# Kernel tuning notes

Hardware: AMD Instinct MI355X
Metric: run time of the kernel (lower is better)

The kernel has to match this reference:

```python
import jax, jax.numpy as jnp
import numpy as np

N, E, D, H = 100000, 1600000, 128, 2
D2 = D * H  # conv2 output dim = out_dim * heads = 256


def setup_inputs() -> dict:
    key = jax.random.key(0)
    ks = jax.random.split(key, 9)
    x = jax.random.normal(ks[0], (N, D), dtype=jnp.float32)
    edge_index = jax.random.randint(ks[1], (2, E), 0, N, dtype=jnp.int64)
    edge_weight = jax.random.uniform(ks[2], (E,), dtype=jnp.float32)
    s = 1.0 / np.sqrt(D)
    W_rel1 = jax.random.normal(ks[3], (D, D), dtype=jnp.float32) * s
    W_root1 = jax.random.normal(ks[4], (D, D), dtype=jnp.float32) * s
    b1 = jnp.zeros((D,), dtype=jnp.float32)
    W_rel2 = jax.random.normal(ks[5], (D, D2), dtype=jnp.float32) * s
    W_root2 = jax.random.normal(ks[6], (D, D2), dtype=jnp.float32) * s
    b2 = jnp.zeros((D2,), dtype=jnp.float32)
    return {"x": x, "edge_index": edge_index, "edge_weight": edge_weight,
            "W_rel1": W_rel1, "b1": b1, "W_root1": W_root1,
            "W_rel2": W_rel2, "b2": b2, "W_root2": W_root2}


def _graph_conv(x, src, dst, edge_weight, W_rel, b, W_root, n_nodes):
    # message: w_e * x_src ; aggregate: mean over incoming edges at dst
    msgs = x[src] * edge_weight[:, None]                       # [E, D]
    summed = jax.ops.segment_sum(msgs, dst, num_segments=n_nodes)  # [N, D]
    cnt = jax.ops.segment_sum(jnp.ones((src.shape[0],), x.dtype), dst,
                              num_segments=n_nodes)
    mean = summed / jnp.maximum(cnt, 1.0)[:, None]
    # GraphConv: lin_rel(aggr) + lin_root(x); bias only on lin_rel
    return mean @ W_rel + b + x @ W_root


def reference(x, edge_index, edge_weight, W_rel1, b1, W_root1, W_rel2, b2, W_root2):
    src, dst = edge_index[0], edge_index[1]
    n = x.shape[0]
    h = _graph_conv(x, src, dst, edge_weight, W_rel1, b1, W_root1, n)
    out = _graph_conv(h, src, dst, edge_weight, W_rel2, b2, W_root2, n)
    return out
```

## Files before the change

### kernel.cpp

```cpp
#include <hip/hip_runtime.h>
#include <hip/hip_bf16.h>

#define D_IN 128
#define SORT_CHUNK 4096
#define NBUCK 256

typedef __attribute__((ext_vector_type(8))) short bf16x8;
typedef __attribute__((ext_vector_type(8))) unsigned short u16x8;
typedef __attribute__((ext_vector_type(4))) float f32x4;


__global__ __launch_bounds__(256) void scan_block_sums(const int* __restrict__ in,
                                                       int* __restrict__ partial,
                                                       int M) {
    __shared__ int sdata[256];
    int b = blockIdx.x, t = threadIdx.x;
    int base = b * 1024 + t * 4;
    int s = 0;
#pragma unroll
    for (int i = 0; i < 4; ++i) {
        int idx = base + i;
        if (idx < M) s += in[idx];
    }
    sdata[t] = s;
    __syncthreads();
    for (int off = 128; off > 0; off >>= 1) {
        if (t < off) sdata[t] += sdata[t + off];
        __syncthreads();
    }
    if (t == 0) partial[b] = sdata[0];
}

__global__ void scan_partials(int* __restrict__ partial, int nb) {
    if (threadIdx.x == 0 && blockIdx.x == 0) {
        int run = 0;
        for (int i = 0; i < nb; ++i) {
            int t = partial[i];
            partial[i] = run;
            run += t;
        }
    }
}

__global__ __launch_bounds__(256) void scan_final(const int* __restrict__ in,
                                                  const int* __restrict__ partial,
                                                  int* __restrict__ outS,
                                                  int M) {
    __shared__ int sdata[256];
    int b = blockIdx.x, t = threadIdx.x;
    int base = b * 1024 + t * 4;
    int v[4];
    int s = 0;
#pragma unroll
    for (int i = 0; i < 4; ++i) {
        int idx = base + i;
        v[i] = (idx < M) ? in[idx] : 0;
        s += v[i];
    }
    sdata[t] = s;
    __syncthreads();
    for (int o = 1; o < 256; o <<= 1) {
        int tmp = 0;
        if (t >= o) tmp = sdata[t - o];
        __syncthreads();
        sdata[t] += tmp;
        __syncthreads();
    }
    int run = partial[b] + (sdata[t] - s);
#pragma unroll
    for (int i = 0; i < 4; ++i) {
        int idx = base + i;
        if (idx < M) outS[idx] = run;
        run += v[i];
    }
}


__global__ __launch_bounds__(256) void bucket_hist_kernel(const int* __restrict__ dst,
                                                          int* __restrict__ bh,
                                                          long long E, int N, int nbe) {
    __shared__ int cnt[NBUCK];
    cnt[threadIdx.x] = 0;
    __syncthreads();
    long long base = (long long)blockIdx.x * SORT_CHUNK;
    long long end = base + SORT_CHUNK;
    if (end > E) end = E;
    for (long long i = base + threadIdx.x; i < end; i += 256) {
        int b = (int)(((long long)dst[i] << 8) / N);
        atomicAdd(&cnt[b], 1);
    }
    __syncthreads();
    bh[threadIdx.x * nbe + blockIdx.x] = cnt[threadIdx.x];
}

__global__ __launch_bounds__(256) void bucket_scatter_kernel(const int* __restrict__ src,
                                                             const int* __restrict__ dst,
                                                             const float* __restrict__ ew,
                                                             const int* __restrict__ S,
                                                             int2* __restrict__ tmp_edges,
                                                             int* __restrict__ tmp_dst,
                                                             long long E, int N, int nbe) {
    __shared__ int base_lds[NBUCK];
    __shared__ int cnt[NBUCK];
    base_lds[threadIdx.x] = S[threadIdx.x * nbe + blockIdx.x];
    cnt[threadIdx.x] = 0;
    __syncthreads();
    long long b0 = (long long)blockIdx.x * SORT_CHUNK;
    long long e1 = b0 + SORT_CHUNK;
    if (e1 > E) e1 = E;
    for (long long i = b0 + threadIdx.x; i < e1; i += 256) {
        int d = dst[i];
        int b = (int)(((long long)d << 8) / N);
        int p = base_lds[b] + atomicAdd(&cnt[b], 1);
        tmp_edges[p] = make_int2(src[i], __float_as_int(ew[i]));
        tmp_dst[p] = d;
    }
}

__global__ __launch_bounds__(256) void bucket_sort_kernel(const int* __restrict__ S,
                                                          const int2* __restrict__ tmp_edges,
                                                          const int* __restrict__ tmp_dst,
                                                          int2* __restrict__ edges,
                                                          int* __restrict__ hist,
                                                          int* __restrict__ off,
                                                          long long E, int N, int nbe) {
    __shared__ int cnt[512];
    __shared__ int tsum[256];
    __shared__ int pos[512];
    const int b = blockIdx.x, t = threadIdx.x;
    const int lo = (int)(((long long)b * N + 255) >> 8);
    const int hi = (int)(((long long)(b + 1) * N + 255) >> 8);
    const int start = S[b * nbe];
    const int end = (b == NBUCK - 1) ? (int)E : S[(b + 1) * nbe];

    cnt[t] = 0;
    cnt[t + 256] = 0;
    __syncthreads();
    for (int i = start + t; i < end; i += 256)
        atomicAdd(&cnt[tmp_dst[i] - lo], 1);
    __syncthreads();

    int a0 = cnt[2 * t], a1 = cnt[2 * t + 1];
    tsum[t] = a0 + a1;
    __syncthreads();
    for (int o = 1; o < 256; o <<= 1) {
        int v = (t >= o) ? tsum[t - o] : 0;
        __syncthreads();
        tsum[t] += v;
        __syncthreads();
    }
    int excl = tsum[t] - (a0 + a1);
    pos[2 * t]     = start + excl;
    pos[2 * t + 1] = start + excl + a0;

    int d0 = lo + 2 * t, d1 = lo + 2 * t + 1;
    if (d0 < hi) { hist[d0] = a0; off[d0] = start + excl + a0; }
    if (d1 < hi) { hist[d1] = a1; off[d1] = start + excl + a0 + a1; }
    __syncthreads();

    for (int i = start + t; i < end; i += 256) {
        int d = tmp_dst[i] - lo;
        int r = atomicAdd(&pos[d], 1);
        edges[r] = tmp_edges[i];
    }
}


__global__ __launch_bounds__(256) void conv_x_kernel(const float* __restrict__ x,
                                                     __hip_bfloat16* __restrict__ xb,
                                                     long long total4) {
    long long i = (long long)blockIdx.x * 256 + threadIdx.x;
    if (i >= total4) return;
    float4 v = reinterpret_cast<const float4*>(x)[i];
    union { ushort4 u; __hip_bfloat162 h2[2]; } o;
    o.h2[0] = __float22bfloat162_rn(make_float2(v.x, v.y));
    o.h2[1] = __float22bfloat162_rn(make_float2(v.z, v.w));
    reinterpret_cast<ushort4*>(xb)[i] = o.u;
}

template <int DOUT>
__global__ __launch_bounds__(256) void conv_w_kernel(const float* __restrict__ Wrel,
                                                     const float* __restrict__ Wroot,
                                                     __hip_bfloat16* __restrict__ Wt) {
    int idx = blockIdx.x * 256 + threadIdx.x;
    if (idx >= DOUT * 256) return;
    int j = idx >> 8;
    int k = idx & 255;
    float v = (k < 128) ? Wrel[(size_t)k * DOUT + j] : Wroot[(size_t)(k - 128) * DOUT + j];
    Wt[idx] = __float2bfloat16(v);
}

__global__ __launch_bounds__(256) void aggregate_kernel(const __hip_bfloat16* __restrict__ featb,
                                                        const int2* __restrict__ edges,
                                                        const int* __restrict__ off,
                                                        const int* __restrict__ hist,
                                                        __hip_bfloat16* __restrict__ aggb,
                                                        int N) {
    int node = blockIdx.x * 4 + (threadIdx.x >> 6);
    if (node >= N) return;
    const int lane = threadIdx.x & 63;
    const int g = lane >> 4;
    const int sub = lane & 15;
    const int cnt = hist[node];
    const int end = off[node];
    const int start = end - cnt;
    const float inv = 1.0f / fmaxf((float)cnt, 1.0f);

    const ushort* fb = (const ushort*)featb;
    float acc[8] = {0.f, 0.f, 0.f, 0.f, 0.f, 0.f, 0.f, 0.f};

    int e = start + g;
    for (; e + 4 < end; e += 8) {
        int2 e0 = edges[e];
        int2 e1 = edges[e + 4];
        float w0 = __int_as_float(e0.y);
        float w1 = __int_as_float(e1.y);
        u16x8 r0 = *reinterpret_cast<const u16x8*>(fb + (size_t)e0.x * 128 + sub * 8);
        u16x8 r1 = *reinterpret_cast<const u16x8*>(fb + (size_t)e1.x * 128 + sub * 8);
#pragma unroll
        for (int j = 0; j < 8; ++j) {
            acc[j] += w0 * __int_as_float((unsigned)r0[j] << 16)
                    + w1 * __int_as_float((unsigned)r1[j] << 16);
        }
    }
    if (e < end) {
        int2 e0 = edges[e];
        float w0 = __int_as_float(e0.y);
        u16x8 r0 = *reinterpret_cast<const u16x8*>(fb + (size_t)e0.x * 128 + sub * 8);
#pragma unroll
        for (int j = 0; j < 8; ++j)
            acc[j] += w0 * __int_as_float((unsigned)r0[j] << 16);
    }

#pragma unroll
    for (int j = 0; j < 8; ++j) {
        acc[j] += __shfl_xor(acc[j], 16, 64);
        acc[j] += __shfl_xor(acc[j], 32, 64);
    }

    if (g == 0) {
        union { u16x8 u; __hip_bfloat162 h2[4]; } o;
#pragma unroll
        for (int j = 0; j < 4; ++j)
            o.h2[j] = __float22bfloat162_rn(make_float2(acc[2 * j] * inv, acc[2 * j + 1] * inv));
        *reinterpret_cast<u16x8*>((ushort*)aggb + (size_t)node * 128 + sub * 8) = o.u;
    }
}

template <int DOUT, bool OUT_BF16>
__global__ __launch_bounds__(256) void gemm_mfma2(const __hip_bfloat16* __restrict__ Arel,
                                                  const __hip_bfloat16* __restrict__ Aroot,
                                                  const __hip_bfloat16* __restrict__ Wt,
                                                  const float* __restrict__ bias,
                                                  void* __restrict__ outp,
                                                  int M) {
    constexpr int NY = DOUT / 128;
    const int nb = gridDim.x;
    const int orig = blockIdx.x;
    const int xcd = orig & 7;
    const int lid = orig >> 3;
    const int q = nb >> 3, r = nb & 7;
    const int wgid = (xcd < r ? xcd * (q + 1) : r * (q + 1) + (xcd - r) * q) + lid;

    const int ty = wgid % NY;
    const int tx = wgid / NY;
    const int tid = threadIdx.x;
    const int lane = tid & 63;
    const int wave = tid >> 6;
    const int lr = lane & 15;
    const int lk = lane >> 4;
    const int mbase = tx * 128 + (wave >> 1) * 64;
    const int nbase = ty * 128 + (wave & 1) * 64;

    const short* arow[4];
    const short* xrow[4];
#pragma unroll
    for (int mi = 0; mi < 4; ++mi) {
        int row = mbase + mi * 16 + lr;
        int rc = row < M ? row : M - 1;
        arow[mi] = (const short*)Arel  + (size_t)rc * 128 + lk * 8;
        xrow[mi] = (const short*)Aroot + (size_t)rc * 128 + lk * 8;
    }
    const short* wrow[4];
#pragma unroll
    for (int ni = 0; ni < 4; ++ni)
        wrow[ni] = (const short*)Wt + (size_t)(nbase + ni * 16 + lr) * 256 + lk * 8;

    f32x4 zero = {0.f, 0.f, 0.f, 0.f};
    f32x4 acc[4][4];
#pragma unroll
    for (int mi = 0; mi < 4; ++mi)
#pragma unroll
        for (int ni = 0; ni < 4; ++ni) acc[mi][ni] = zero;

#pragma unroll
    for (int kk = 0; kk < 8; ++kk) {
        bf16x8 a[4], b[4];
#pragma unroll
        for (int mi = 0; mi < 4; ++mi)
            a[mi] = (kk < 4)
                ? *reinterpret_cast<const bf16x8*>(arow[mi] + kk * 32)
                : *reinterpret_cast<const bf16x8*>(xrow[mi] + (kk - 4) * 32);
#pragma unroll
        for (int ni = 0; ni < 4; ++ni)
            b[ni] = *reinterpret_cast<const bf16x8*>(wrow[ni] + kk * 32);
#pragma unroll
        for (int mi = 0; mi < 4; ++mi)
#pragma unroll
            for (int ni = 0; ni < 4; ++ni)
                acc[mi][ni] = __builtin_amdgcn_mfma_f32_16x16x32_bf16(a[mi], b[ni], acc[mi][ni], 0, 0, 0);
    }

#pragma unroll
    for (int mi = 0; mi < 4; ++mi)
#pragma unroll
        for (int ni = 0; ni < 4; ++ni) {
            int col = nbase + ni * 16 + lr;
            float bv = bias[col];
#pragma unroll
            for (int rr = 0; rr < 4; ++rr) {
                int row = mbase + mi * 16 + lk * 4 + rr;
                if (row < M) {
                    float v = acc[mi][ni][rr] + bv;
                    if (OUT_BF16)
                        ((__hip_bfloat16*)outp)[(size_t)row * DOUT + col] = __float2bfloat16(v);
                    else
                        __builtin_nontemporal_store(v, (float*)outp + (size_t)row * DOUT + col);
                }
            }
        }
}


extern "C" void kernel_launch(void* const* d_in, const int* in_sizes, int n_in,
                              void* d_out, int out_size, void* d_ws, size_t ws_size,
                              hipStream_t stream) {
    const float* x      = (const float*)d_in[0];
    const int*   ei     = (const int*)d_in[1];
    const float* ew     = (const float*)d_in[2];
    const float* Wrel1  = (const float*)d_in[3];
    const float* b1     = (const float*)d_in[4];
    const float* Wroot1 = (const float*)d_in[5];
    const float* Wrel2  = (const float*)d_in[6];
    const float* b2     = (const float*)d_in[7];
    const float* Wroot2 = (const float*)d_in[8];
    float* out = (float*)d_out;

    const int N = in_sizes[0] / D_IN;
    const long long E = in_sizes[2];
    const int* src = ei;
    const int* dst = ei + E;

    const int nbe = (int)((E + SORT_CHUNK - 1) / SORT_CHUNK);
    const int M = nbe * NBUCK;
    const int nbM = (M + 1023) / 1024;

    int* hist = (int*)d_ws;
    int* off  = hist + N;
    int* part = off + N;
    int2* edges = (int2*)(part + 128);
    __hip_bfloat16* agg1b = (__hip_bfloat16*)(edges + E);
    __hip_bfloat16* xb    = agg1b + (size_t)N * D_IN;
    __hip_bfloat16* agg2b = xb    + (size_t)N * D_IN;
    __hip_bfloat16* hb    = agg2b + (size_t)N * D_IN;
    __hip_bfloat16* Wt1   = hb    + (size_t)N * D_IN;
    __hip_bfloat16* Wt2   = Wt1   + 128 * 256;

    int* bh      = (int*)agg1b;
    int* S       = bh + M;
    int* tmp_dst = S + M;
    int2* tmp_edges = (int2*)agg2b;

    bucket_hist_kernel<<<nbe, 256, 0, stream>>>(dst, bh, E, N, nbe);
    scan_block_sums<<<nbM, 256, 0, stream>>>(bh, part, M);
    scan_partials<<<1, 64, 0, stream>>>(part, nbM);
    scan_final<<<nbM, 256, 0, stream>>>(bh, part, S, M);
    bucket_scatter_kernel<<<nbe, 256, 0, stream>>>(src, dst, ew, S, tmp_edges, tmp_dst, E, N, nbe);
    bucket_sort_kernel<<<NBUCK, 256, 0, stream>>>(S, tmp_edges, tmp_dst, edges, hist, off, E, N, nbe);

    {
        long long total4 = (long long)N * D_IN / 4;
        conv_x_kernel<<<(int)((total4 + 255) / 256), 256, 0, stream>>>(x, xb, total4);
        conv_w_kernel<128><<<(128 * 256 + 255) / 256, 256, 0, stream>>>(Wrel1, Wroot1, Wt1);
        conv_w_kernel<256><<<(256 * 256 + 255) / 256, 256, 0, stream>>>(Wrel2, Wroot2, Wt2);
    }

    const int ab = (N + 3) / 4;
    const int gx = (N + 127) / 128;

    aggregate_kernel<<<ab, 256, 0, stream>>>(xb, edges, off, hist, agg1b, N);
    gemm_mfma2<128, true><<<gx * 1, 256, 0, stream>>>(agg1b, xb, Wt1, b1, hb, N);

    aggregate_kernel<<<ab, 256, 0, stream>>>(hb, edges, off, hist, agg2b, N);
    gemm_mfma2<256, false><<<gx * 2, 256, 0, stream>>>(agg2b, hb, Wt2, b2, out, N);
}
```

Before: 331.6 us.

## Stage GEMM weight tile in swizzled LDS and prefetch all A fragments

The GEMM kernel now copies its 128-column weight slice (64 KB) into shared memory with direct global-to-LDS loads, using an XOR swizzle to avoid bank conflicts, and reads B fragments from LDS instead of from global memory per wave. It also loads all eight K-steps of A fragments into registers before the MFMA loop so the loads can be issued together. In exchange, each block needs 64 KB of LDS and many more registers, which may cap occupancy at two blocks per CU as the launch bound states.

Result: faster. 300.0 us (-9.5%).

```diff
diff --git a/kernel.cpp b/kernel.cpp
--- a/kernel.cpp
+++ b/kernel.cpp
@@ -248,13 +248,15 @@
 }
 
 template <int DOUT, bool OUT_BF16>
-__global__ __launch_bounds__(256) void gemm_mfma2(const __hip_bfloat16* __restrict__ Arel,
-                                                  const __hip_bfloat16* __restrict__ Aroot,
-                                                  const __hip_bfloat16* __restrict__ Wt,
-                                                  const float* __restrict__ bias,
-                                                  void* __restrict__ outp,
-                                                  int M) {
+__global__ __launch_bounds__(256, 2) void gemm_mfma4(const __hip_bfloat16* __restrict__ Arel,
+                                                     const __hip_bfloat16* __restrict__ Aroot,
+                                                     const __hip_bfloat16* __restrict__ Wt,
+                                                     const float* __restrict__ bias,
+                                                     void* __restrict__ outp,
+                                                     int M) {
     constexpr int NY = DOUT / 128;
+    __shared__ __align__(16) unsigned char Bs[65536];
+
     const int nb = gridDim.x;
     const int orig = blockIdx.x;
     const int xcd = orig & 7;
@@ -269,8 +271,23 @@
     const int wave = tid >> 6;
     const int lr = lane & 15;
     const int lk = lane >> 4;
+
+    const char* wbase = (const char*)(Wt + (size_t)ty * 128 * 256);
+#pragma unroll
+    for (int i = 0; i < 16; ++i) {
+        int s = i * 256 + tid;
+        int col = s >> 5;
+        int off16 = s & 31;
+        int g16 = col * 32 + (off16 ^ (col & 7));
+        __builtin_amdgcn_global_load_lds(
+            (const __attribute__((address_space(1))) unsigned int*)(wbase + (size_t)g16 * 16),
+            (__attribute__((address_space(3))) unsigned int*)(&Bs[s * 16]),
+            16, 0, 0);
+    }
+
     const int mbase = tx * 128 + (wave >> 1) * 64;
-    const int nbase = ty * 128 + (wave & 1) * 64;
+    const int nwave = (wave & 1) * 64;
+    const int nbase = ty * 128 + nwave;
 
     const short* arow[4];
     const short* xrow[4];
@@ -281,10 +298,17 @@
         arow[mi] = (const short*)Arel  + (size_t)rc * 128 + lk * 8;
         xrow[mi] = (const short*)Aroot + (size_t)rc * 128 + lk * 8;
     }
-    const short* wrow[4];
-#pragma unroll
-    for (int ni = 0; ni < 4; ++ni)
-        wrow[ni] = (const short*)Wt + (size_t)(nbase + ni * 16 + lr) * 256 + lk * 8;
+
+    __syncthreads();
+
+    bf16x8 abuf[8][4];
+#pragma unroll
+    for (int kk = 0; kk < 8; ++kk)
+#pragma unroll
+        for (int mi = 0; mi < 4; ++mi)
+            abuf[kk][mi] = (kk < 4)
+                ? *reinterpret_cast<const bf16x8*>(arow[mi] + kk * 32)
+                : *reinterpret_cast<const bf16x8*>(xrow[mi] + (kk - 4) * 32);
 
     f32x4 zero = {0.f, 0.f, 0.f, 0.f};
     f32x4 acc[4][4];
@@ -295,20 +319,18 @@
 
 #pragma unroll
     for (int kk = 0; kk < 8; ++kk) {
-        bf16x8 a[4], b[4];
+        bf16x8 b[4];
+#pragma unroll
+        for (int ni = 0; ni < 4; ++ni) {
+            int c = nwave + ni * 16 + lr;
+            int byteoff = c * 512 + ((kk * 64 + lk * 16) ^ ((c & 7) << 4));
+            b[ni] = *reinterpret_cast<const bf16x8*>(&Bs[byteoff]);
+        }
 #pragma unroll
         for (int mi = 0; mi < 4; ++mi)
-            a[mi] = (kk < 4)
-                ? *reinterpret_cast<const bf16x8*>(arow[mi] + kk * 32)
-                : *reinterpret_cast<const bf16x8*>(xrow[mi] + (kk - 4) * 32);
-#pragma unroll
-        for (int ni = 0; ni < 4; ++ni)
-            b[ni] = *reinterpret_cast<const bf16x8*>(wrow[ni] + kk * 32);
-#pragma unroll
-        for (int mi = 0; mi < 4; ++mi)
 #pragma unroll
             for (int ni = 0; ni < 4; ++ni)
-                acc[mi][ni] = __builtin_amdgcn_mfma_f32_16x16x32_bf16(a[mi], b[ni], acc[mi][ni], 0, 0, 0);
+                acc[mi][ni] = __builtin_amdgcn_mfma_f32_16x16x32_bf16(abuf[kk][mi], b[ni], acc[mi][ni], 0, 0, 0);
     }
 
 #pragma unroll
@@ -389,8 +411,8 @@
     const int gx = (N + 127) / 128;
 
     aggregate_kernel<<<ab, 256, 0, stream>>>(xb, edges, off, hist, agg1b, N);
-    gemm_mfma2<128, true><<<gx * 1, 256, 0, stream>>>(agg1b, xb, Wt1, b1, hb, N);
+    gemm_mfma4<128, true><<<gx * 1, 256, 0, stream>>>(agg1b, xb, Wt1, b1, hb, N);
 
     aggregate_kernel<<<ab, 256, 0, stream>>>(hb, edges, off, hist, agg2b, N);
-    gemm_mfma2<256, false><<<gx * 2, 256, 0, stream>>>(agg2b, hb, Wt2, b2, out, N);
-}
+    gemm_mfma4<256, false><<<gx * 2, 256, 0, stream>>>(agg2b, hb, Wt2, b2, out, N);
+}
```

## Stage weight tile in LDS via direct global-to-LDS loads with 512-thread GEMM blocks

Applied to the files above, without the earlier changes.

The weight matrix is re-laid out into per-128-column strips with k-chunk-major slots. Each GEMM block now copies its 64KB weight strip into shared memory using global_load_lds and reads B fragments from LDS instead of global memory. Blocks grow to 512 threads (8 waves, each computing 64x32), which halves per-wave accumulator count. The 64KB of LDS per block limits how many blocks fit on a CU, and every block pays a full-strip load before it can compute.

Measured after the change: 327.3 us. Within noise of the previous version (-1.3%).

```diff
diff --git a/kernel.cpp b/kernel.cpp
--- a/kernel.cpp
+++ b/kernel.cpp
@@ -184,9 +184,16 @@
                                                      __hip_bfloat16* __restrict__ Wt) {
     int idx = blockIdx.x * 256 + threadIdx.x;
     if (idx >= DOUT * 256) return;
-    int j = idx >> 8;
-    int k = idx & 255;
-    float v = (k < 128) ? Wrel[(size_t)k * DOUT + j] : Wroot[(size_t)(k - 128) * DOUT + j];
+    int strip  = idx >> 15;
+    int within = idx & 32767;
+    int s      = within >> 3;
+    int j      = within & 7;
+    int kchunk = s >> 7;
+    int col    = s & 127;
+    int k      = kchunk * 8 + j;
+    int jcol   = strip * 128 + col;
+    float v = (k < 128) ? Wrel[(size_t)k * DOUT + jcol]
+                        : Wroot[(size_t)(k - 128) * DOUT + jcol];
     Wt[idx] = __float2bfloat16(v);
 }
 
@@ -248,13 +255,15 @@
 }
 
 template <int DOUT, bool OUT_BF16>
-__global__ __launch_bounds__(256) void gemm_mfma2(const __hip_bfloat16* __restrict__ Arel,
-                                                  const __hip_bfloat16* __restrict__ Aroot,
-                                                  const __hip_bfloat16* __restrict__ Wt,
-                                                  const float* __restrict__ bias,
-                                                  void* __restrict__ outp,
-                                                  int M) {
+__global__ __launch_bounds__(512, 4) void gemm_mfma5(const __hip_bfloat16* __restrict__ Arel,
+                                                     const __hip_bfloat16* __restrict__ Aroot,
+                                                     const __hip_bfloat16* __restrict__ Wt,
+                                                     const float* __restrict__ bias,
+                                                     void* __restrict__ outp,
+                                                     int M) {
     constexpr int NY = DOUT / 128;
+    __shared__ __align__(16) unsigned char Bs[65536];
+
     const int nb = gridDim.x;
     const int orig = blockIdx.x;
     const int xcd = orig & 7;
@@ -269,8 +278,22 @@
     const int wave = tid >> 6;
     const int lr = lane & 15;
     const int lk = lane >> 4;
-    const int mbase = tx * 128 + (wave >> 1) * 64;
-    const int nbase = ty * 128 + (wave & 1) * 64;
+
+    const char* wbase = (const char*)Wt + (size_t)ty * 65536;
+#pragma unroll
+    for (int i = 0; i < 8; ++i) {
+        int s = i * 512 + tid;
+        __builtin_amdgcn_global_load_lds(
+            (const __attribute__((address_space(1))) unsigned int*)(wbase + (size_t)s * 16),
+            (__attribute__((address_space(3))) unsigned int*)(&Bs[s * 16]),
+            16, 0, 0);
+    }
+
+    const int wr = wave >> 2;
+    const int wc = wave & 3;
+    const int mbase = tx * 128 + wr * 64;
+    const int nloc = wc * 32;
+    const int nbase = ty * 128 + nloc;
 
     const short* arow[4];
     const short* xrow[4];
@@ -281,40 +304,40 @@
         arow[mi] = (const short*)Arel  + (size_t)rc * 128 + lk * 8;
         xrow[mi] = (const short*)Aroot + (size_t)rc * 128 + lk * 8;
     }
-    const short* wrow[4];
-#pragma unroll
-    for (int ni = 0; ni < 4; ++ni)
-        wrow[ni] = (const short*)Wt + (size_t)(nbase + ni * 16 + lr) * 256 + lk * 8;
+
+    __syncthreads();
 
     f32x4 zero = {0.f, 0.f, 0.f, 0.f};
-    f32x4 acc[4][4];
+    f32x4 acc[4][2];
 #pragma unroll
     for (int mi = 0; mi < 4; ++mi)
 #pragma unroll
-        for (int ni = 0; ni < 4; ++ni) acc[mi][ni] = zero;
+        for (int ni = 0; ni < 2; ++ni) acc[mi][ni] = zero;
 
 #pragma unroll
     for (int kk = 0; kk < 8; ++kk) {
-        bf16x8 a[4], b[4];
+        bf16x8 a[4], b[2];
 #pragma unroll
         for (int mi = 0; mi < 4; ++mi)
             a[mi] = (kk < 4)
                 ? *reinterpret_cast<const bf16x8*>(arow[mi] + kk * 32)
                 : *reinterpret_cast<const bf16x8*>(xrow[mi] + (kk - 4) * 32);
 #pragma unroll
-        for (int ni = 0; ni < 4; ++ni)
-            b[ni] = *reinterpret_cast<const bf16x8*>(wrow[ni] + kk * 32);
+        for (int ni = 0; ni < 2; ++ni) {
+            int slot = (kk * 4 + lk) * 128 + nloc + ni * 16 + lr;
+            b[ni] = *reinterpret_cast<const bf16x8*>(&Bs[slot * 16]);
+        }
 #pragma unroll
         for (int mi = 0; mi < 4; ++mi)
 #pragma unroll
-            for (int ni = 0; ni < 4; ++ni)
+            for (int ni = 0; ni < 2; ++ni)
                 acc[mi][ni] = __builtin_amdgcn_mfma_f32_16x16x32_bf16(a[mi], b[ni], acc[mi][ni], 0, 0, 0);
     }
 
 #pragma unroll
     for (int mi = 0; mi < 4; ++mi)
 #pragma unroll
-        for (int ni = 0; ni < 4; ++ni) {
+        for (int ni = 0; ni < 2; ++ni) {
             int col = nbase + ni * 16 + lr;
             float bv = bias[col];
 #pragma unroll
@@ -389,8 +412,8 @@
     const int gx = (N + 127) / 128;
 
     aggregate_kernel<<<ab, 256, 0, stream>>>(xb, edges, off, hist, agg1b, N);
-    gemm_mfma2<128, true><<<gx * 1, 256, 0, stream>>>(agg1b, xb, Wt1, b1, hb, N);
+    gemm_mfma5<128, true><<<gx * 1, 512, 0, stream>>>(agg1b, xb, Wt1, b1, hb, N);
 
     aggregate_kernel<<<ab, 256, 0, stream>>>(hb, edges, off, hist, agg2b, N);
-    gemm_mfma2<256, false><<<gx * 2, 256, 0, stream>>>(agg2b, hb, Wt2, b2, out, N);
-}
+    gemm_mfma5<256, false><<<gx * 2, 512, 0, stream>>>(agg2b, hb, Wt2, b2, out, N);
+}
```
